# Performance work log

Measured on AMD Instinct MI355X. Metric: run time of the kernel, lower is better.

## Reference

```python
import jax, jax.numpy as jnp
import numpy as np

EPS = 1e-05

def _self_cost_cosine(embs):
    # embs: [n, d] -> cost: [n, n]
    energy = jnp.sqrt(jnp.sum(embs ** 2, axis=1, keepdims=True))  # [n,1]
    gram = embs @ embs.T
    denom = energy @ energy.T + EPS
    return 1.0 - jnp.exp(-5.0 * (1.0 - gram / denom))

def _mutual_cost_cosine(embs1, embs2):
    e1 = jnp.sqrt(jnp.sum(embs1 ** 2, axis=1, keepdims=True))
    e2 = jnp.sqrt(jnp.sum(embs2 ** 2, axis=1, keepdims=True))
    gram = embs1 @ embs2.T
    denom = e1 @ e2.T + EPS
    return 1.0 - jnp.exp(-(1.0 - gram / denom))

def _tensor_times_mat_l2(cost_s, cost_t, trans, mu_s, mu_t):
    f1 = (cost_s ** 2) @ mu_s            # [n1,1], broadcasts over columns
    f2 = mu_t.T @ (cost_t ** 2).T        # [1,n2], broadcasts over rows
    return f1 + f2 - 2.0 * (cost_s @ trans @ cost_t.T)

def _similarity_l2(cost_pred, cost_truth):
    return jnp.sum((cost_pred - cost_truth) ** 2 * jnp.exp(-cost_truth))

def _orthogonal(embs):
    d = embs.shape[1]
    orth = embs.T @ embs - jnp.eye(d, dtype=embs.dtype)
    return jnp.sum(orth ** 2)

def setup_inputs() -> dict:
    key = jax.random.key(0)
    ks = jax.random.split(key, 9)
    num1, num2, dim, n = 50000, 50000, 128, 4096
    emb1_w = jax.random.uniform(ks[0], (num1, dim), jnp.float32, -1.0 / dim, 1.0 / dim)
    emb2_w = jax.random.uniform(ks[1], (num2, dim), jnp.float32, -1.0 / dim, 1.0 / dim)
    index1 = jax.random.randint(ks[2], (n,), 0, num1, dtype=jnp.int64 if jax.config.jax_enable_x64 else jnp.int32)
    index2 = jax.random.randint(ks[3], (n,), 0, num2, dtype=jnp.int64 if jax.config.jax_enable_x64 else jnp.int32)
    trans = jax.random.uniform(ks[4], (n, n), jnp.float32) / (n * n)
    mu_s = jax.random.uniform(ks[5], (n, 1), jnp.float32) / n
    mu_t = jax.random.uniform(ks[6], (n, 1), jnp.float32) / n
    cost1 = jax.random.uniform(ks[7], (n, n), jnp.float32)
    cost2 = jax.random.uniform(ks[8], (n, n), jnp.float32)
    return {"index1": index1, "index2": index2, "trans": trans, "mu_s": mu_s,
            "mu_t": mu_t, "cost1": cost1, "cost2": cost2,
            "emb1_w": emb1_w, "emb2_w": emb2_w}

def reference(index1, index2, trans, mu_s, mu_t, cost1, cost2, emb1_w, emb2_w):
    embs1 = emb1_w[index1]  # [n1, d]
    embs2 = emb2_w[index2]  # [n2, d]
    cost_s = _self_cost_cosine(embs1)
    cost_t = _self_cost_cosine(embs2)
    cost_st = _mutual_cost_cosine(embs1, embs2)
    cost = _tensor_times_mat_l2(cost_s, cost_t, trans, mu_s, mu_t)
    d_gw = jnp.sum(cost * trans)
    d_w = jnp.sum(cost_st * trans)
    regularizer = (_similarity_l2(cost_s, cost1) + _similarity_l2(cost_t, cost2)
                   + _orthogonal(embs1) + _orthogonal(embs2))
    return (d_gw, d_w, regularizer)
```

## Files before the change

kernel.cpp:

```cpp
#include <hip/hip_runtime.h>
#include <math.h>

#define N 4096
#define D 128
#define FEPS 1e-5f
#define C0F 0.993262053f

typedef __attribute__((ext_vector_type(8))) short bf16x8;
typedef __attribute__((ext_vector_type(4))) float f32x4;

__device__ __forceinline__ unsigned short f2bf(float f) {
    union { float f; unsigned u; } v; v.f = f;
    unsigned r = v.u + 0x7fffu + ((v.u >> 16) & 1u);
    return (unsigned short)(r >> 16);
}
__device__ __forceinline__ float bf2f(short s) {
    union { unsigned u; float f; } v; v.u = ((unsigned)(unsigned short)s) << 16;
    return v.f;
}

__device__ __forceinline__ void async16(void* lds, const void* g) {
    __builtin_amdgcn_global_load_lds(
        (const __attribute__((address_space(1))) unsigned int*)g,
        (__attribute__((address_space(3))) unsigned int*)lds, 16, 0, 0);
}

__device__ __forceinline__ double block_reduce256(double v, double* red) {
    int t = threadIdx.x;
    red[t] = v;
    __syncthreads();
    #pragma unroll
    for (int s = 128; s > 0; s >>= 1) {
        if (t < s) red[t] += red[t + s];
        __syncthreads();
    }
    double r = red[0];
    __syncthreads();
    return r;
}

__global__ void gather_energy(const float* __restrict__ W, const int* __restrict__ idx,
                              float* __restrict__ E, float* __restrict__ energy) {
    int i = blockIdx.x, t = threadIdx.x;
    float v = W[(size_t)idx[i] * D + t];
    E[(size_t)i * D + t] = v;
    float sq = v * v;
    #pragma unroll
    for (int o = 32; o > 0; o >>= 1) sq += __shfl_down(sq, o);
    __shared__ float s2[2];
    if ((t & 63) == 0) s2[t >> 6] = sq;
    __syncthreads();
    if (t == 0) energy[i] = sqrtf(s2[0] + s2[1]);
}

__global__ void trans_convert(const float* __restrict__ T,
                              unsigned short* __restrict__ Ta,
                              unsigned short* __restrict__ Tb,
                              float* __restrict__ trow, float* __restrict__ tcol,
                              double* __restrict__ sc) {
    __shared__ float cs[4][256];
    __shared__ float ws[4];
    int t = threadIdx.x;
    int cb = blockIdx.x * 64 + (t & 63);
    int rb = blockIdx.y * 4 + (t >> 6);
    int r0 = rb * 4, c0 = cb * 4;
    float vv[4][4];
    #pragma unroll
    for (int i = 0; i < 4; ++i) {
        float4 r4 = *(const float4*)&T[(size_t)(r0 + i) * N + c0];
        vv[i][0] = r4.x; vv[i][1] = r4.y; vv[i][2] = r4.z; vv[i][3] = r4.w;
    }
    #pragma unroll
    for (int i = 0; i < 4; ++i) {
        int r = r0 + i;
        size_t slot = ((size_t)(r >> 4) * (N / 8) + (c0 >> 3)) * 128 + (r & 15) * 8 + (c0 & 7);
        short4 s;
        s.x = (short)f2bf(vv[i][0]); s.y = (short)f2bf(vv[i][1]);
        s.z = (short)f2bf(vv[i][2]); s.w = (short)f2bf(vv[i][3]);
        *(short4*)&Ta[slot] = s;
    }
    #pragma unroll
    for (int j = 0; j < 4; ++j) {
        int n = c0 + j;
        size_t slot = ((size_t)(n >> 4) * (N / 8) + (r0 >> 3)) * 128 + (n & 15) * 8 + (r0 & 7);
        short4 s;
        s.x = (short)f2bf(vv[0][j]); s.y = (short)f2bf(vv[1][j]);
        s.z = (short)f2bf(vv[2][j]); s.w = (short)f2bf(vv[3][j]);
        *(short4*)&Tb[slot] = s;
    }
    float wtot = 0.f;
    #pragma unroll
    for (int i = 0; i < 4; ++i) {
        float s = vv[i][0] + vv[i][1] + vv[i][2] + vv[i][3];
        #pragma unroll
        for (int o = 32; o > 0; o >>= 1) s += __shfl_down(s, o);
        if ((t & 63) == 0) { atomicAdd(&trow[r0 + i], s); wtot += s; }
    }
    if ((t & 63) == 0) ws[t >> 6] = wtot;
    int g = t >> 6;
    #pragma unroll
    for (int j = 0; j < 4; ++j)
        cs[g][(t & 63) * 4 + j] = vv[0][j] + vv[1][j] + vv[2][j] + vv[3][j];
    __syncthreads();
    float csum = cs[0][t] + cs[1][t] + cs[2][t] + cs[3][t];
    atomicAdd(&tcol[blockIdx.x * 256 + t], csum);
    if (t == 0) atomicAdd(&sc[5], (double)(ws[0] + ws[1] + ws[2] + ws[3]));
}

template <int SELF>
__global__ __launch_bounds__(256) void cost_kernel(
        const float* __restrict__ EA, const float* __restrict__ EB,
        const float* __restrict__ ea, const float* __restrict__ eb,
        const float* __restrict__ ref_or_trans,
        const float* __restrict__ mu, const float* __restrict__ tsum,
        unsigned short* __restrict__ outD, double* __restrict__ sc) {
    __shared__ float As[16][68];
    __shared__ float Bs[16][68];
    __shared__ double red[256];
    int t = threadIdx.x;
    int tx = t & 15, ty = t >> 4;
    int bi = blockIdx.y * 64, bj = blockIdx.x * 64;
    float acc[4][4] = {};
    for (int kk = 0; kk < D; kk += 16) {
        #pragma unroll
        for (int r = 0; r < 4; ++r) {
            int e = t + 256 * r;
            int ar = e >> 4, ac = e & 15;
            As[ac][ar] = EA[(size_t)(bi + ar) * D + kk + ac];
            Bs[ac][ar] = EB[(size_t)(bj + ar) * D + kk + ac];
        }
        __syncthreads();
        #pragma unroll
        for (int k = 0; k < 16; ++k) {
            float4 av = *(const float4*)&As[k][ty * 4];
            float4 bv = *(const float4*)&Bs[k][tx * 4];
            float a[4] = {av.x, av.y, av.z, av.w};
            float b[4] = {bv.x, bv.y, bv.z, bv.w};
            #pragma unroll
            for (int u = 0; u < 4; ++u)
                #pragma unroll
                for (int v = 0; v < 4; ++v)
                    acc[u][v] = fmaf(a[u], b[v], acc[u][v]);
        }
        __syncthreads();
    }
    float eav[4], ebv[4];
    #pragma unroll
    for (int u = 0; u < 4; ++u) eav[u] = ea[bi + ty * 4 + u];
    #pragma unroll
    for (int v = 0; v < 4; ++v) ebv[v] = eb[bj + tx * 4 + v];

    double l1 = 0.0, l2 = 0.0;
    #pragma unroll
    for (int u = 0; u < 4; ++u) {
        int ri = bi + ty * 4 + u;
        float cv[4];
        #pragma unroll
        for (int v = 0; v < 4; ++v) {
            int ci = bj + tx * 4 + v;
            size_t id = (size_t)ri * N + ci;
            float denom = eav[u] * ebv[v] + FEPS;
            float cosv = acc[u][v] / denom;
            if (SELF) {
                float c = 1.f - expf(-5.f * (1.f - cosv));
                cv[v] = c;
                float rc = ref_or_trans[id];
                float dd = c - rc;
                l1 += (double)(dd * dd * expf(-rc));
                l2 += (double)(c * c) * (double)mu[ci] * (double)tsum[ri];
            } else {
                float c = 1.f - expf(-(1.f - cosv));
                l1 += (double)c * (double)ref_or_trans[id];
            }
        }
        if (SELF) {
            int ci0 = bj + tx * 4;
            size_t slot = ((size_t)(ri >> 4) * (N / 8) + (ci0 >> 3)) * 128 + (ri & 15) * 8 + (ci0 & 7);
            short4 s;
            s.x = (short)f2bf(cv[0] - C0F); s.y = (short)f2bf(cv[1] - C0F);
            s.z = (short)f2bf(cv[2] - C0F); s.w = (short)f2bf(cv[3] - C0F);
            *(short4*)&outD[slot] = s;
        }
    }
    double s1 = block_reduce256(l1, red);
    if (SELF) {
        double s2v = block_reduce256(l2, red);
        if (t == 0) { atomicAdd(&sc[0], s1); atomicAdd(&sc[1], s2v); }
    } else {
        if (t == 0) atomicAdd(&sc[3], s1);
    }
}

__device__ __forceinline__ void mfma_step(const char* ard, const char* brd,
                                          f32x4 (&acc)[4][4]) {
    bf16x8 af[4], bfr[4];
    #pragma unroll
    for (int f = 0; f < 4; ++f) {
        af[f]  = *(const bf16x8*)(ard + f * 1024);
        bfr[f] = *(const bf16x8*)(brd + f * 1024);
    }
    #pragma unroll
    for (int mf = 0; mf < 4; ++mf)
        #pragma unroll
        for (int nf = 0; nf < 4; ++nf)
            acc[mf][nf] = __builtin_amdgcn_mfma_f32_16x16x32_bf16(
                af[mf], bfr[nf], acc[mf][nf], 0, 0, 0);
}

template <int STORE>
__global__ __launch_bounds__(256, 3) void gemm_mfma(
        const unsigned short* __restrict__ Ag, const unsigned short* __restrict__ Bg,
        unsigned short* __restrict__ Pdb,
        const float* __restrict__ trow, const float* __restrict__ tcol,
        double* __restrict__ sc) {
    __shared__ __align__(16) char Abuf[2][8192];
    __shared__ __align__(16) char Bbuf[2][8192];
    __shared__ double red[256];
    const int t = threadIdx.x, l = t & 63;
    const int w = __builtin_amdgcn_readfirstlane(t >> 6);
    const int wm = w >> 1, wn = w & 1;
    const int lid = blockIdx.x;
    const int by = (lid & 7) * 4 + ((lid >> 3) & 3);
    const int bx = lid >> 5;
    const size_t grp = (size_t)(N / 8) * 256;

    const char* aG = (const char*)Ag + (size_t)(by * 8 + w * 2) * grp + (size_t)(l * 16);
    const char* bG = (const char*)Bg + (size_t)(bx * 8 + w * 2) * grp + (size_t)(l * 16);

    f32x4 acc[4][4];
    #pragma unroll
    for (int i = 0; i < 4; ++i)
        #pragma unroll
        for (int j = 0; j < 4; ++j)
            acc[i][j] = (f32x4){0.f, 0.f, 0.f, 0.f};

    async16(&Abuf[0][w * 2048],        aG);
    async16(&Abuf[0][w * 2048 + 1024], aG + grp);
    async16(&Bbuf[0][w * 2048],        bG);
    async16(&Bbuf[0][w * 2048 + 1024], bG + grp);

    for (int it = 0; it < N / 32; ++it) {
        __syncthreads();
        const int ph = it & 1, pn = ph ^ 1;
        if (it + 1 < N / 32) {
            const char* a = aG + (size_t)(it + 1) * 1024;
            const char* b = bG + (size_t)(it + 1) * 1024;
            async16(&Abuf[pn][w * 2048],        a);
            async16(&Abuf[pn][w * 2048 + 1024], a + grp);
            async16(&Bbuf[pn][w * 2048],        b);
            async16(&Bbuf[pn][w * 2048 + 1024], b + grp);
        }
        mfma_step(&Abuf[ph][wm * 4096] + l * 16, &Bbuf[ph][wn * 4096] + l * 16, acc);
    }

    const size_t blkbase = (size_t)(by * 32 + bx) * 4096 + (size_t)w * 1024;
    if (STORE) {
        #pragma unroll
        for (int mf = 0; mf < 4; ++mf)
            #pragma unroll
            for (int nf = 0; nf < 4; ++nf) {
                f32x4 a = acc[mf][nf];
                short4 s;
                s.x = (short)f2bf(a[0]); s.y = (short)f2bf(a[1]);
                s.z = (short)f2bf(a[2]); s.w = (short)f2bf(a[3]);
                *(short4*)&Pdb[(blkbase + (mf * 4 + nf) * 64 + l) * 4] = s;
            }
    } else {
        double t1 = 0.0, t2 = 0.0, t3 = 0.0;
        const int quad = l >> 4, lan = l & 15;
        #pragma unroll
        for (int mf = 0; mf < 4; ++mf) {
            const int ib = by * 128 + wm * 64 + mf * 16 + quad * 4;
            float4 tr4 = *(const float4*)&trow[ib];
            float trv[4] = {tr4.x, tr4.y, tr4.z, tr4.w};
            #pragma unroll
            for (int nf = 0; nf < 4; ++nf) {
                const int j = bx * 128 + wn * 64 + nf * 16 + lan;
                const float tcj = tcol[j];
                short4 p = *(const short4*)&Pdb[(blkbase + (mf * 4 + nf) * 64 + l) * 4];
                float pf[4] = {bf2f(p.x), bf2f(p.y), bf2f(p.z), bf2f(p.w)};
                #pragma unroll
                for (int r = 0; r < 4; ++r) {
                    double x = (double)acc[mf][nf][r];
                    t1 += (double)tcj * x;
                    t2 += (double)trv[r] * (double)pf[r];
                    t3 += x * (double)pf[r];
                }
            }
        }
        double s1 = block_reduce256(t1, red);
        double s2 = block_reduce256(t2, red);
        double s3 = block_reduce256(t3, red);
        if (t == 0) {
            atomicAdd(&sc[6], s1);
            atomicAdd(&sc[7], s2);
            atomicAdd(&sc[2], s3);
        }
    }
}

__global__ __launch_bounds__(256) void gram_partial(const float* __restrict__ E,
                                                    float* __restrict__ G) {
    __shared__ float Es[16][132];
    int t = threadIdx.x, tx = t & 15, ty = t >> 4;
    int i0 = blockIdx.x * 128;
    float acc[8][8] = {};
    for (int kk = 0; kk < 128; kk += 16) {
        #pragma unroll
        for (int r = 0; r < 2; ++r) {
            int q = t + 256 * r;
            int row = q >> 5, c4 = (q & 31) * 4;
            *(float4*)&Es[row][c4] = *(const float4*)&E[(size_t)(i0 + kk + row) * D + c4];
        }
        __syncthreads();
        #pragma unroll
        for (int k = 0; k < 16; ++k) {
            float a[8], b[8];
            *(float4*)&a[0] = *(const float4*)&Es[k][ty * 8];
            *(float4*)&a[4] = *(const float4*)&Es[k][ty * 8 + 4];
            *(float4*)&b[0] = *(const float4*)&Es[k][tx * 8];
            *(float4*)&b[4] = *(const float4*)&Es[k][tx * 8 + 4];
            #pragma unroll
            for (int u = 0; u < 8; ++u)
                #pragma unroll
                for (int v = 0; v < 8; ++v)
                    acc[u][v] = fmaf(a[u], b[v], acc[u][v]);
        }
        __syncthreads();
    }
    #pragma unroll
    for (int u = 0; u < 8; ++u)
        #pragma unroll
        for (int v = 0; v < 8; ++v)
            atomicAdd(&G[(size_t)(ty * 8 + u) * D + tx * 8 + v], acc[u][v]);
}

__global__ void orth_final(const float* __restrict__ G, double* __restrict__ sc) {
    __shared__ double red[256];
    const float* g = G + (size_t)blockIdx.x * D * D;
    int t = threadIdx.x;
    double s = 0.0;
    for (int q = t; q < D * D; q += 256) {
        float v = g[q] - ((q % (D + 1)) == 0 ? 1.f : 0.f);
        s += (double)v * (double)v;
    }
    double r = block_reduce256(s, red);
    if (t == 0) atomicAdd(&sc[4], r);
}

__global__ void finalize(const double* __restrict__ sc, float* __restrict__ out) {
    if (threadIdx.x == 0) {
        const double C0 = (double)C0F;
        double S = sc[5];
        double pq = C0 * C0 * S * S + C0 * sc[6] + C0 * sc[7] + sc[2];
        out[0] = (float)(sc[1] - 2.0 * pq);
        out[1] = (float)sc[3];
        out[2] = (float)(sc[0] + sc[4]);
    }
}

extern "C" void kernel_launch(void* const* d_in, const int* in_sizes, int n_in,
                              void* d_out, int out_size, void* d_ws, size_t ws_size,
                              hipStream_t stream) {
    const int*   index1 = (const int*)d_in[0];
    const int*   index2 = (const int*)d_in[1];
    const float* trans  = (const float*)d_in[2];
    const float* mu_s   = (const float*)d_in[3];
    const float* mu_t   = (const float*)d_in[4];
    const float* cost1  = (const float*)d_in[5];
    const float* cost2  = (const float*)d_in[6];
    const float* emb1_w = (const float*)d_in[7];
    const float* emb2_w = (const float*)d_in[8];
    float* out = (float*)d_out;

    char* w = (char*)d_ws;
    double* sc  = (double*)w;
    float* tcol = (float*)(w + 256);
    float* trow = (float*)(w + 16640);
    float* e1   = (float*)(w + 33024);
    float* e2   = (float*)(w + 49408);
    float* E1   = (float*)(w + 65792);
    float* E2   = (float*)(w + 2162944);
    unsigned short* Ds  = (unsigned short*)(w + 4260096);
    unsigned short* Ta  = (unsigned short*)(w + 37814528);
    unsigned short* Tb  = (unsigned short*)(w + 71368960);
    unsigned short* Pdb = (unsigned short*)(w + 104923392);
    float* Gbuf = (float*)(w + 37814528);

    hipMemsetAsync(d_ws, 0, 33024, stream);

    gather_energy<<<N, D, 0, stream>>>(emb1_w, index1, E1, e1);
    gather_energy<<<N, D, 0, stream>>>(emb2_w, index2, E2, e2);
    trans_convert<<<dim3(16, 256), 256, 0, stream>>>(trans, Ta, Tb, trow, tcol, sc);

    dim3 g64(N / 64, N / 64);

    cost_kernel<1><<<g64, 256, 0, stream>>>(E1, E1, e1, e1, cost1, mu_s, trow, Ds, sc);
    gemm_mfma<1><<<1024, 256, 0, stream>>>(Ds, Tb, Pdb, nullptr, nullptr, sc);
    cost_kernel<1><<<g64, 256, 0, stream>>>(E2, E2, e2, e2, cost2, mu_t, tcol, Ds, sc);
    gemm_mfma<0><<<1024, 256, 0, stream>>>(Ta, Ds, Pdb, trow, tcol, sc);
    cost_kernel<0><<<g64, 256, 0, stream>>>(E1, E2, e1, e2, trans, nullptr, nullptr, nullptr, sc);
    hipMemsetAsync(Gbuf, 0, 2 * D * D * sizeof(float), stream);
    gram_partial<<<32, 256, 0, stream>>>(E1, Gbuf);
    gram_partial<<<32, 256, 0, stream>>>(E2, Gbuf + D * D);
    orth_final<<<2, 256, 0, stream>>>(Gbuf, sc);

    finalize<<<1, 64, 0, stream>>>(sc, out);
}
```

Measured before the change: 1.024 ms.

## Enlarge GEMM tiles to 256x256 with 8 waves and phased async pipeline

```diff
diff --git a/kernel.cpp b/kernel.cpp
--- a/kernel.cpp
+++ b/kernel.cpp
@@ -5,6 +5,7 @@
 #define D 128
 #define FEPS 1e-5f
 #define C0F 0.993262053f
+#define NT 64
 
 typedef __attribute__((ext_vector_type(8))) short bf16x8;
 typedef __attribute__((ext_vector_type(4))) float f32x4;
@@ -31,6 +32,20 @@
     __syncthreads();
     #pragma unroll
     for (int s = 128; s > 0; s >>= 1) {
+        if (t < s) red[t] += red[t + s];
+        __syncthreads();
+    }
+    double r = red[0];
+    __syncthreads();
+    return r;
+}
+
+__device__ __forceinline__ double block_reduce512(double v, double* red) {
+    int t = threadIdx.x;
+    red[t] = v;
+    __syncthreads();
+    #pragma unroll
+    for (int s = 256; s > 0; s >>= 1) {
         if (t < s) red[t] += red[t + s];
         __syncthreads();
     }
@@ -191,93 +206,159 @@
     }
 }
 
-__device__ __forceinline__ void mfma_step(const char* ard, const char* brd,
-                                          f32x4 (&acc)[4][4]) {
-    bf16x8 af[4], bfr[4];
-    #pragma unroll
-    for (int f = 0; f < 4; ++f) {
-        af[f]  = *(const bf16x8*)(ard + f * 1024);
-        bfr[f] = *(const bf16x8*)(brd + f * 1024);
-    }
-    #pragma unroll
-    for (int mf = 0; mf < 4; ++mf)
-        #pragma unroll
-        for (int nf = 0; nf < 4; ++nf)
-            acc[mf][nf] = __builtin_amdgcn_mfma_f32_16x16x32_bf16(
-                af[mf], bfr[nf], acc[mf][nf], 0, 0, 0);
-}
+#define MFMA16(a, b, c) __builtin_amdgcn_mfma_f32_16x16x32_bf16(a, b, c, 0, 0, 0)
 
 template <int STORE>
-__global__ __launch_bounds__(256, 3) void gemm_mfma(
+__global__ __launch_bounds__(512, 2) void gemm_mfma(
         const unsigned short* __restrict__ Ag, const unsigned short* __restrict__ Bg,
         unsigned short* __restrict__ Pdb,
         const float* __restrict__ trow, const float* __restrict__ tcol,
         double* __restrict__ sc) {
-    __shared__ __align__(16) char Abuf[2][8192];
-    __shared__ __align__(16) char Bbuf[2][8192];
-    __shared__ double red[256];
+    __shared__ __align__(16) char Lds[131072];
+    __shared__ double red[512];
     const int t = threadIdx.x, l = t & 63;
     const int w = __builtin_amdgcn_readfirstlane(t >> 6);
-    const int wm = w >> 1, wn = w & 1;
+    const int wm = w >> 2, wn = w & 3;
     const int lid = blockIdx.x;
-    const int by = (lid & 7) * 4 + ((lid >> 3) & 3);
-    const int bx = lid >> 5;
-    const size_t grp = (size_t)(N / 8) * 256;
-
-    const char* aG = (const char*)Ag + (size_t)(by * 8 + w * 2) * grp + (size_t)(l * 16);
-    const char* bG = (const char*)Bg + (size_t)(bx * 8 + w * 2) * grp + (size_t)(l * 16);
-
-    f32x4 acc[4][4];
-    #pragma unroll
-    for (int i = 0; i < 4; ++i)
+    const int swz = (lid & 7) * 32 + (lid >> 3);
+    const int by = swz >> 4, bx = swz & 15;
+    const size_t GRP = (size_t)(N / 8) * 256;
+
+    const char* aBase = (const char*)Ag + ((size_t)by * 16 + w) * GRP + (size_t)l * 16;
+    const char* bBase = (const char*)Bg + ((size_t)bx * 16 + w) * GRP + (size_t)l * 16;
+
+#define ISSUE_A(KH, TT) do {                                                   \
+    char* _d = Lds + ((TT) & 1) * 65536 + (KH) * 16384 + w * 1024;             \
+    const char* _g = aBase + (size_t)(TT) * 2048 + (KH) * 1024;                \
+    async16(_d, _g); async16(_d + 8192, _g + 8 * GRP); } while (0)
+#define ISSUE_B(KH, TT) do {                                                   \
+    char* _d = Lds + ((TT) & 1) * 65536 + 32768 + (KH) * 16384 + w * 1024;     \
+    const char* _g = bBase + (size_t)(TT) * 2048 + (KH) * 1024;                \
+    async16(_d, _g); async16(_d + 8192, _g + 8 * GRP); } while (0)
+
+    f32x4 acc[8][4];
+    #pragma unroll
+    for (int i = 0; i < 8; ++i)
         #pragma unroll
         for (int j = 0; j < 4; ++j)
             acc[i][j] = (f32x4){0.f, 0.f, 0.f, 0.f};
 
-    async16(&Abuf[0][w * 2048],        aG);
-    async16(&Abuf[0][w * 2048 + 1024], aG + grp);
-    async16(&Bbuf[0][w * 2048],        bG);
-    async16(&Bbuf[0][w * 2048 + 1024], bG + grp);
-
-    for (int it = 0; it < N / 32; ++it) {
-        __syncthreads();
-        const int ph = it & 1, pn = ph ^ 1;
-        if (it + 1 < N / 32) {
-            const char* a = aG + (size_t)(it + 1) * 1024;
-            const char* b = bG + (size_t)(it + 1) * 1024;
-            async16(&Abuf[pn][w * 2048],        a);
-            async16(&Abuf[pn][w * 2048 + 1024], a + grp);
-            async16(&Bbuf[pn][w * 2048],        b);
-            async16(&Bbuf[pn][w * 2048 + 1024], b + grp);
-        }
-        mfma_step(&Abuf[ph][wm * 4096] + l * 16, &Bbuf[ph][wn * 4096] + l * 16, acc);
-    }
-
-    const size_t blkbase = (size_t)(by * 32 + bx) * 4096 + (size_t)w * 1024;
+    ISSUE_A(0, 0); ISSUE_B(0, 0); ISSUE_A(1, 0); ISSUE_B(1, 0); ISSUE_A(0, 1);
+    asm volatile("s_waitcnt vmcnt(6)" ::: "memory");
+    __builtin_amdgcn_s_barrier();
+    asm volatile("" ::: "memory");
+
+    bf16x8 af[8];
+    const char* Albase = Lds + wm * 8192;
+    const char* Blbase = Lds + 32768 + wn * 4096;
+
+    for (int tt = 0; tt < NT; ++tt) {
+        const int bufo = (tt & 1) * 65536;
+        {
+            const char* Ab = Albase + bufo;
+            const char* Bb = Blbase + bufo;
+            #pragma unroll
+            for (int mf = 0; mf < 8; ++mf)
+                af[mf] = *(const bf16x8*)(Ab + mf * 1024 + l * 16);
+            bf16x8 b0 = *(const bf16x8*)(Bb + l * 16);
+            bf16x8 b1 = *(const bf16x8*)(Bb + 1024 + l * 16);
+            if (tt + 1 < NT) ISSUE_B(0, tt + 1);
+            __builtin_amdgcn_s_setprio(1);
+            #pragma unroll
+            for (int mf = 0; mf < 8; ++mf) {
+                acc[mf][0] = MFMA16(af[mf], b0, acc[mf][0]);
+                acc[mf][1] = MFMA16(af[mf], b1, acc[mf][1]);
+            }
+            __builtin_amdgcn_s_setprio(0);
+            asm volatile("" ::: "memory");
+            __builtin_amdgcn_s_barrier();
+            asm volatile("" ::: "memory");
+        }
+        {
+            const char* Bb = Blbase + bufo + 2048;
+            bf16x8 b0 = *(const bf16x8*)(Bb + l * 16);
+            bf16x8 b1 = *(const bf16x8*)(Bb + 1024 + l * 16);
+            if (tt + 1 < NT) ISSUE_A(1, tt + 1);
+            __builtin_amdgcn_s_setprio(1);
+            #pragma unroll
+            for (int mf = 0; mf < 8; ++mf) {
+                acc[mf][2] = MFMA16(af[mf], b0, acc[mf][2]);
+                acc[mf][3] = MFMA16(af[mf], b1, acc[mf][3]);
+            }
+            __builtin_amdgcn_s_setprio(0);
+            if (tt < NT - 1) { asm volatile("s_waitcnt vmcnt(6)" ::: "memory"); }
+            else             { asm volatile("s_waitcnt vmcnt(0)" ::: "memory"); }
+            asm volatile("" ::: "memory");
+            __builtin_amdgcn_s_barrier();
+            asm volatile("" ::: "memory");
+        }
+        {
+            const char* Ab = Albase + bufo + 16384;
+            const char* Bb = Blbase + bufo + 16384;
+            #pragma unroll
+            for (int mf = 0; mf < 8; ++mf)
+                af[mf] = *(const bf16x8*)(Ab + mf * 1024 + l * 16);
+            bf16x8 b0 = *(const bf16x8*)(Bb + l * 16);
+            bf16x8 b1 = *(const bf16x8*)(Bb + 1024 + l * 16);
+            if (tt + 1 < NT) ISSUE_B(1, tt + 1);
+            __builtin_amdgcn_s_setprio(1);
+            #pragma unroll
+            for (int mf = 0; mf < 8; ++mf) {
+                acc[mf][0] = MFMA16(af[mf], b0, acc[mf][0]);
+                acc[mf][1] = MFMA16(af[mf], b1, acc[mf][1]);
+            }
+            __builtin_amdgcn_s_setprio(0);
+            asm volatile("" ::: "memory");
+            __builtin_amdgcn_s_barrier();
+            asm volatile("" ::: "memory");
+        }
+        {
+            const char* Bb = Blbase + bufo + 16384 + 2048;
+            bf16x8 b0 = *(const bf16x8*)(Bb + l * 16);
+            bf16x8 b1 = *(const bf16x8*)(Bb + 1024 + l * 16);
+            if (tt + 2 < NT) ISSUE_A(0, tt + 2);
+            __builtin_amdgcn_s_setprio(1);
+            #pragma unroll
+            for (int mf = 0; mf < 8; ++mf) {
+                acc[mf][2] = MFMA16(af[mf], b0, acc[mf][2]);
+                acc[mf][3] = MFMA16(af[mf], b1, acc[mf][3]);
+            }
+            __builtin_amdgcn_s_setprio(0);
+            if (tt < NT - 2)       { asm volatile("s_waitcnt vmcnt(6)" ::: "memory"); }
+            else if (tt == NT - 2) { asm volatile("s_waitcnt vmcnt(4)" ::: "memory"); }
+            asm volatile("" ::: "memory");
+            __builtin_amdgcn_s_barrier();
+            asm volatile("" ::: "memory");
+        }
+    }
+#undef ISSUE_A
+#undef ISSUE_B
+
+    const size_t base = ((size_t)(by * 16 + bx)) * 65536 + (size_t)w * 8192;
     if (STORE) {
         #pragma unroll
-        for (int mf = 0; mf < 4; ++mf)
+        for (int mf = 0; mf < 8; ++mf)
             #pragma unroll
             for (int nf = 0; nf < 4; ++nf) {
                 f32x4 a = acc[mf][nf];
                 short4 s;
                 s.x = (short)f2bf(a[0]); s.y = (short)f2bf(a[1]);
                 s.z = (short)f2bf(a[2]); s.w = (short)f2bf(a[3]);
-                *(short4*)&Pdb[(blkbase + (mf * 4 + nf) * 64 + l) * 4] = s;
+                *(short4*)&Pdb[base + (size_t)(mf * 4 + nf) * 256 + (size_t)l * 4] = s;
             }
     } else {
         double t1 = 0.0, t2 = 0.0, t3 = 0.0;
         const int quad = l >> 4, lan = l & 15;
         #pragma unroll
-        for (int mf = 0; mf < 4; ++mf) {
-            const int ib = by * 128 + wm * 64 + mf * 16 + quad * 4;
+        for (int mf = 0; mf < 8; ++mf) {
+            const int ib = by * 256 + wm * 128 + mf * 16 + quad * 4;
             float4 tr4 = *(const float4*)&trow[ib];
             float trv[4] = {tr4.x, tr4.y, tr4.z, tr4.w};
             #pragma unroll
             for (int nf = 0; nf < 4; ++nf) {
-                const int j = bx * 128 + wn * 64 + nf * 16 + lan;
+                const int j = bx * 256 + wn * 64 + nf * 16 + lan;
                 const float tcj = tcol[j];
-                short4 p = *(const short4*)&Pdb[(blkbase + (mf * 4 + nf) * 64 + l) * 4];
+                short4 p = *(const short4*)&Pdb[base + (size_t)(mf * 4 + nf) * 256 + (size_t)l * 4];
                 float pf[4] = {bf2f(p.x), bf2f(p.y), bf2f(p.z), bf2f(p.w)};
                 #pragma unroll
                 for (int r = 0; r < 4; ++r) {
@@ -288,9 +369,9 @@
                 }
             }
         }
-        double s1 = block_reduce256(t1, red);
-        double s2 = block_reduce256(t2, red);
-        double s3 = block_reduce256(t3, red);
+        double s1 = block_reduce512(t1, red);
+        double s2 = block_reduce512(t2, red);
+        double s3 = block_reduce512(t3, red);
         if (t == 0) {
             atomicAdd(&sc[6], s1);
             atomicAdd(&sc[7], s2);
@@ -396,9 +477,9 @@
     dim3 g64(N / 64, N / 64);
 
     cost_kernel<1><<<g64, 256, 0, stream>>>(E1, E1, e1, e1, cost1, mu_s, trow, Ds, sc);
-    gemm_mfma<1><<<1024, 256, 0, stream>>>(Ds, Tb, Pdb, nullptr, nullptr, sc);
+    gemm_mfma<1><<<256, 512, 0, stream>>>(Ds, Tb, Pdb, nullptr, nullptr, sc);
     cost_kernel<1><<<g64, 256, 0, stream>>>(E2, E2, e2, e2, cost2, mu_t, tcol, Ds, sc);
-    gemm_mfma<0><<<1024, 256, 0, stream>>>(Ta, Ds, Pdb, trow, tcol, sc);
+    gemm_mfma<0><<<256, 512, 0, stream>>>(Ta, Ds, Pdb, trow, tcol, sc);
     cost_kernel<0><<<g64, 256, 0, stream>>>(E1, E2, e1, e2, trans, nullptr, nullptr, nullptr, sc);
     hipMemsetAsync(Gbuf, 0, 2 * D * D * sizeof(float), stream);
     gram_partial<<<32, 256, 0, stream>>>(E1, Gbuf);
```

Result: faster. 954.9 us (-6.7%).
